# Kernel optimization log

Hardware: AMD Instinct MI355X
Metric: run time of the kernel (lower is better)

Reference implementation:

```python
import jax, jax.numpy as jnp
import numpy as np

# Fixed architecture constants (match init_kwargs)
D_MODEL = 256
NHEAD = 8
BASE_WINDOW = 4
DFF = 1024
B = 1
S = 4096


def _win_idx(grid, w):
    """Token indices of overlapping w x w windows over a grid x grid image,
    stride w//2 (same windows as F.unfold(kernel=w, stride=w//2)). -> (L, w*w) int32."""
    s = w // 2
    starts = np.arange(0, grid - w + 1, s)
    rows = starts[:, None] + np.arange(w)[None, :]              # (n, w)
    idx = rows[:, None, :, None] * grid + rows[None, :, None, :]  # (n, n, w, w)
    return jnp.asarray(idx.reshape(-1, w * w), dtype=jnp.int32)


def _ln(x, g, b, eps=1e-5):
    m = jnp.mean(x, axis=-1, keepdims=True)
    v = jnp.var(x, axis=-1, keepdims=True)
    return (x - m) * jax.lax.rsqrt(v + eps) * g + b


def _local_attn(x, scale, fw, fb, fg, fbb):
    """Multi-scale windowed SDPA: gather windows, attend, mean-pool per window,
    scatter pooled features back to token positions (overlap-averaged), fuse."""
    Bq, Sq, Dm = x.shape
    grid = int(np.sqrt(Sq))
    inv_scale = 1.0 / float(np.sqrt(Dm))  # SDPA uses full D as head dim
    outs = []
    for i in range(3):
        w = BASE_WINDOW * (2 ** i) * scale
        idx = _win_idx(grid, w)                      # (L, w2)
        win = x[:, idx, :]                           # (B, L, w2, D) gather
        p = jax.nn.softmax(jnp.einsum('blqd,blkd->blqk', win, win) * inv_scale, axis=-1)
        pooled = jnp.einsum('blqk,blkd->blqd', p, win).mean(axis=2)  # (B, L, D)
        flat = idx.reshape(-1)
        contrib = jnp.broadcast_to(pooled[:, :, None, :], win.shape).reshape(Bq, -1, Dm)
        acc = jnp.zeros_like(x).at[:, flat, :].add(contrib)
        cnt = jnp.zeros((Sq,), x.dtype).at[flat].add(1.0)
        outs.append(acc / cnt[None, :, None])        # (B, S, D) per scale
    cat = jnp.concatenate(outs, axis=-1)             # (B, S, 3D)
    return _ln(cat @ fw + fb, fg, fbb)


def _mha(x, wq, wk, wv, bq, bk, bv, wo, bo):
    Bq, Sq, Dm = x.shape
    dh = Dm // NHEAD
    def split(t):
        return t.reshape(Bq, Sq, NHEAD, dh)
    q, k, v = split(x @ wq + bq), split(x @ wk + bk), split(x @ wv + bv)
    p = jax.nn.softmax(jnp.einsum('bqhd,bkhd->bhqk', q, k) * (1.0 / float(np.sqrt(dh))), axis=-1)
    o = jnp.einsum('bhqk,bkhd->bqhd', p, v).reshape(Bq, Sq, Dm)
    return o @ wo + bo


def _forward(x, pos, fw, fb, fg, fbb, wq, wk, wv, bq, bk, bv, wo, bo, gw, gb, w1, b1, w2, b2, n1g, n1b, n2g, n2b, n3g, n3b, local_scale):
    # pos is accepted but unused in the original math (device check only)
    xl = _local_attn(x, local_scale, fw, fb, fg, fbb)
    xl = _ln(x + xl, n1g, n1b)                 # norm1 residual (dropout is identity in eval)
    xg = _mha(xl, wq, wk, wv, bq, bk, bv, wo, bo)
    xg = _ln(xl + xg, n2g, n2b)                # norm2 residual
    gate = jax.nn.softmax(((xl + xg) * 0.5).mean(axis=1, keepdims=True) @ gw + gb, axis=-1)  # (B,1,2)
    alpha, beta = gate[..., 0:1], gate[..., 1:2]
    xf = alpha * xg + beta * xl
    ff = jax.nn.gelu(xf @ w1 + b1, approximate=False) @ w2 + b2
    return _ln(xf + ff, n3g, n3b)


def setup_inputs() -> dict:
    key = jax.random.key(0)
    ks = jax.random.split(key, 12)
    def rn(k, shape, s=0.02):
        return jax.random.normal(k, shape, jnp.float32) * s
    D = D_MODEL
    return {
        'x': jax.random.normal(ks[0], (B, S, D), jnp.float32),
        'pos': jax.random.normal(ks[1], (B, S, 2), jnp.float32),
        'fw': rn(ks[2], (3 * D, D)), 'fb': jnp.zeros((D,), jnp.float32),
        'fg': jnp.ones((D,), jnp.float32), 'fbb': jnp.zeros((D,), jnp.float32),
        'wq': rn(ks[3], (D, D)), 'wk': rn(ks[4], (D, D)), 'wv': rn(ks[5], (D, D)),
        'bq': jnp.zeros((D,), jnp.float32), 'bk': jnp.zeros((D,), jnp.float32), 'bv': jnp.zeros((D,), jnp.float32),
        'wo': rn(ks[6], (D, D)), 'bo': jnp.zeros((D,), jnp.float32),
        'gw': rn(ks[7], (D, 2)), 'gb': jnp.zeros((2,), jnp.float32),
        'w1': rn(ks[8], (D, DFF)), 'b1': jnp.zeros((DFF,), jnp.float32),
        'w2': rn(ks[9], (DFF, D)), 'b2': jnp.zeros((D,), jnp.float32),
        'n1g': jnp.ones((D,), jnp.float32), 'n1b': jnp.zeros((D,), jnp.float32),
        'n2g': jnp.ones((D,), jnp.float32), 'n2b': jnp.zeros((D,), jnp.float32),
        'n3g': jnp.ones((D,), jnp.float32), 'n3b': jnp.zeros((D,), jnp.float32),
        'local_scale': 1,
    }


def reference(x, pos, fw, fb, fg, fbb, wq, wk, wv, bq, bk, bv, wo, bo, gw, gb, w1, b1, w2, b2, n1g, n1b, n2g, n2b, n3g, n3b, local_scale):
    return _forward(x, pos, fw, fb, fg, fbb, wq, wk, wv, bq, bk, bv, wo, bo, gw, gb, w1, b1, w2, b2, n1g, n1b, n2g, n2b, n3g, n3b, local_scale)
```

## Files before the change

kernel.cpp:

```cpp
#include <hip/hip_runtime.h>
#include <cstdint>
#include <cstddef>


#define DEVFN __device__ __forceinline__

constexpr int S    = 4096;
constexpr int D    = 256;
constexpr int GRID = 64;
constexpr int NH   = 8;
constexpr int DH   = 32;

typedef __attribute__((ext_vector_type(8))) short bf16x8;
typedef __attribute__((ext_vector_type(4))) float f32x4;
typedef __attribute__((ext_vector_type(16))) float f32x16;
typedef __attribute__((ext_vector_type(2))) unsigned int u32x2;

DEVFN float asf(unsigned u) { return __uint_as_float(u); }

DEVFN unsigned short f2bf(float f) {
  unsigned u = __float_as_uint(f);
  u += 0x7fffu + ((u >> 16) & 1u);
  return (unsigned short)(u >> 16);
}
DEVFN float bf2f(unsigned short s) { return __uint_as_float(((unsigned)s) << 16); }

DEVFN bf16x8 pack8(float4 a, float4 b) {
  bf16x8 kv;
  kv[0] = (short)f2bf(a.x); kv[1] = (short)f2bf(a.y);
  kv[2] = (short)f2bf(a.z); kv[3] = (short)f2bf(a.w);
  kv[4] = (short)f2bf(b.x); kv[5] = (short)f2bf(b.y);
  kv[6] = (short)f2bf(b.z); kv[7] = (short)f2bf(b.w);
  return kv;
}

DEVFN float gelu_t(float u) {
  const float y = 0.7978845608028654f * (u + 0.044715f * u * u * u);
  const float e = __expf(2.f * y);
  return 0.5f * u * (2.f - 2.f / (e + 1.f));
}

__global__ __launch_bounds__(256) void k_wt(
    const float* fw, const float* wq, const float* wk, const float* wv,
    const float* wo, const float* w1, const float* w2,
    unsigned short* fwT, unsigned short* wqT, unsigned short* wkT,
    unsigned short* wvT, unsigned short* woT, unsigned short* w1T,
    unsigned short* w2T) {
  __shared__ unsigned short tile[32][36];
  const int bid = blockIdx.x;
  const float* src; unsigned short* dst; int K, N, t;
  if (bid < 192)      { src = fw; dst = fwT; K = 768;  N = 256;  t = bid; }
  else if (bid < 256) { src = wq; dst = wqT; K = 256;  N = 256;  t = bid - 192; }
  else if (bid < 320) { src = wk; dst = wkT; K = 256;  N = 256;  t = bid - 256; }
  else if (bid < 384) { src = wv; dst = wvT; K = 256;  N = 256;  t = bid - 320; }
  else if (bid < 448) { src = wo; dst = woT; K = 256;  N = 256;  t = bid - 384; }
  else if (bid < 704) { src = w1; dst = w1T; K = 256;  N = 1024; t = bid - 448; }
  else                { src = w2; dst = w2T; K = 1024; N = 256;  t = bid - 704; }
  const int nkt = K >> 5;
  const int k0 = (t % nkt) * 32, n0 = (t / nkt) * 32;
  const int i = threadIdx.x >> 3, j4 = threadIdx.x & 7;
  const float4 v = *(const float4*)(src + (size_t)(k0 + i) * N + n0 + j4 * 4);
  unsigned lo = (unsigned)f2bf(v.x) | ((unsigned)f2bf(v.y) << 16);
  unsigned hi = (unsigned)f2bf(v.z) | ((unsigned)f2bf(v.w) << 16);
  *(uint2*)&tile[i][j4 * 4] = make_uint2(lo, hi);
  __syncthreads();
  unsigned o0 = tile[j4 * 4 + 0][i], o1 = tile[j4 * 4 + 1][i];
  unsigned o2 = tile[j4 * 4 + 2][i], o3 = tile[j4 * 4 + 3][i];
  *(uint2*)(dst + (size_t)(n0 + i) * K + k0 + j4 * 4) =
      make_uint2(o0 | (o1 << 16), o2 | (o3 << 16));
}

template <int K, int OUTBF, int ACT>
__global__ __launch_bounds__(64) void k_gemm_m(const unsigned short* __restrict__ Ab,
                                               const unsigned short* __restrict__ WT,
                                               const float* __restrict__ bias,
                                               void* __restrict__ Cout, int N) {
  const int lane = threadIdx.x;
  const int lc = lane & 31, hi = lane >> 5;
  const int m0 = blockIdx.x * 32, n0 = blockIdx.y * 32;
  const unsigned short* ap = Ab + (size_t)(m0 + lc) * K + hi * 8;
  const unsigned short* bp = WT + (size_t)(n0 + lc) * K + hi * 8;
  f32x16 acc = {0.f,0.f,0.f,0.f,0.f,0.f,0.f,0.f,0.f,0.f,0.f,0.f,0.f,0.f,0.f,0.f};
#pragma unroll 4
  for (int k0 = 0; k0 < K; k0 += 16) {
    bf16x8 a = *(const bf16x8*)(ap + k0);
    bf16x8 b = *(const bf16x8*)(bp + k0);
    acc = __builtin_amdgcn_mfma_f32_32x32x16_bf16(a, b, acc, 0, 0, 0);
  }
  const float bv = bias[n0 + lc];
#pragma unroll
  for (int r = 0; r < 16; ++r) {
    const int row = (r & 3) + 8 * (r >> 2) + 4 * hi;
    float v = acc[r] + bv;
    if (ACT == 1) v = gelu_t(v);
    if (OUTBF) ((unsigned short*)Cout)[(size_t)(m0 + row) * N + n0 + lc] = f2bf(v);
    else       ((float*)Cout)[(size_t)(m0 + row) * N + n0 + lc] = v;
  }
}

__global__ __launch_bounds__(64) void k_gemm_qkv(const unsigned short* __restrict__ Ab,
                                                 const unsigned short* __restrict__ wqkvT,
                                                 const float* __restrict__ bq,
                                                 const float* __restrict__ bk,
                                                 const float* __restrict__ bv,
                                                 unsigned short* __restrict__ qb,
                                                 unsigned short* __restrict__ kb,
                                                 unsigned short* __restrict__ vb) {
  const int lane = threadIdx.x;
  const int lc = lane & 31, hi = lane >> 5;
  const int m0 = blockIdx.x * 32;
  const int sel = blockIdx.y >> 3, n0 = (blockIdx.y & 7) * 32;
  const unsigned short* WT = wqkvT + (size_t)sel * 256 * 256;
  const float* bias = sel == 0 ? bq : sel == 1 ? bk : bv;
  unsigned short* out = sel == 0 ? qb : sel == 1 ? kb : vb;
  const float oscale = sel == 0 ? 0.17677669529663687f : 1.f;
  const unsigned short* ap = Ab + (size_t)(m0 + lc) * 256 + hi * 8;
  const unsigned short* bp = WT + (size_t)(n0 + lc) * 256 + hi * 8;
  f32x16 acc = {0.f,0.f,0.f,0.f,0.f,0.f,0.f,0.f,0.f,0.f,0.f,0.f,0.f,0.f,0.f,0.f};
#pragma unroll 4
  for (int k0 = 0; k0 < 256; k0 += 16) {
    bf16x8 a = *(const bf16x8*)(ap + k0);
    bf16x8 b = *(const bf16x8*)(bp + k0);
    acc = __builtin_amdgcn_mfma_f32_32x32x16_bf16(a, b, acc, 0, 0, 0);
  }
  const float bvv = bias[n0 + lc];
#pragma unroll
  for (int r = 0; r < 16; ++r) {
    const int row = (r & 3) + 8 * (r >> 2) + 4 * hi;
    out[(size_t)(m0 + row) * 256 + n0 + lc] = f2bf((acc[r] + bvv) * oscale);
  }
}

template <int W, int THREADS>
__global__ __launch_bounds__(THREADS) void k_local_s(const float* __restrict__ x,
                                                     float* __restrict__ pooled, int nS) {
  constexpr int NT  = W * W;
  constexpr int NCT = NT / 16;
  constexpr int LDE = 264;
  __shared__ unsigned short win[NT][LDE];
  __shared__ float a[NT];
  const int tid = threadIdx.x;
  const int wave = tid >> 6, lane = tid & 63;
  const int lr = lane & 15, lg = lane >> 4;
  const int l = blockIdx.x;
  const int row0 = (l / nS) * (W / 2), col0 = (l % nS) * (W / 2);

  for (int e8 = tid; e8 < NT * 32; e8 += THREADS) {
    const int t = e8 >> 5, c8 = (e8 & 31) * 8;
    const float* src = x + ((size_t)((row0 + t / W) * GRID + col0 + (t % W))) * D + c8;
    *(bf16x8*)&win[t][c8] = pack8(*(const float4*)src, *(const float4*)(src + 4));
  }
  if (tid < NT) a[tid] = 0.f;
  __syncthreads();

  bf16x8 af[8];
#pragma unroll
  for (int k2 = 0; k2 < 8; ++k2)
    af[k2] = *(const bf16x8*)&win[wave * 16 + lr][k2 * 32 + lg * 8];

  float m[4], Z[4], Zi[4];
#pragma unroll
  for (int r = 0; r < 4; ++r) { m[r] = -INFINITY; Z[r] = 0.f; }

  for (int ct = 0; ct < NCT; ++ct) {
    f32x4 Ca = {0.f, 0.f, 0.f, 0.f}, Cb = {0.f, 0.f, 0.f, 0.f};
#pragma unroll
    for (int k2 = 0; k2 < 8; k2 += 2) {
      bf16x8 b0 = *(const bf16x8*)&win[ct * 16 + lr][k2 * 32 + lg * 8];
      bf16x8 b1 = *(const bf16x8*)&win[ct * 16 + lr][(k2 + 1) * 32 + lg * 8];
      Ca = __builtin_amdgcn_mfma_f32_16x16x32_bf16(af[k2], b0, Ca, 0, 0, 0);
      Cb = __builtin_amdgcn_mfma_f32_16x16x32_bf16(af[k2 + 1], b1, Cb, 0, 0, 0);
    }
#pragma unroll
    for (int r = 0; r < 4; ++r) {
      const float sv = (Ca[r] + Cb[r]) * 0.0625f;
      const float nm = fmaxf(m[r], sv);
      Z[r] = Z[r] * __expf(m[r] - nm) + __expf(sv - nm);
      m[r] = nm;
    }
  }
#pragma unroll
  for (int r = 0; r < 4; ++r) {
#pragma unroll
    for (int msk = 1; msk <= 8; msk <<= 1) {
      const float om = __shfl_xor(m[r], msk), oz = __shfl_xor(Z[r], msk);
      const float nm = fmaxf(m[r], om);
      Z[r] = Z[r] * __expf(m[r] - nm) + oz * __expf(om - nm);
      m[r] = nm;
    }
    Zi[r] = 1.f / Z[r];
  }

  for (int ct = 0; ct < NCT; ++ct) {
    f32x4 Ca = {0.f, 0.f, 0.f, 0.f}, Cb = {0.f, 0.f, 0.f, 0.f};
#pragma unroll
    for (int k2 = 0; k2 < 8; k2 += 2) {
      bf16x8 b0 = *(const bf16x8*)&win[ct * 16 + lr][k2 * 32 + lg * 8];
      bf16x8 b1 = *(const bf16x8*)&win[ct * 16 + lr][(k2 + 1) * 32 + lg * 8];
      Ca = __builtin_amdgcn_mfma_f32_16x16x32_bf16(af[k2], b0, Ca, 0, 0, 0);
      Cb = __builtin_amdgcn_mfma_f32_16x16x32_bf16(af[k2 + 1], b1, Cb, 0, 0, 0);
    }
    float cs = 0.f;
#pragma unroll
    for (int r = 0; r < 4; ++r)
      cs += __expf((Ca[r] + Cb[r]) * 0.0625f - m[r]) * Zi[r];
    cs += __shfl_xor(cs, 16);
    cs += __shfl_xor(cs, 32);
    if (lg == 0) atomicAdd(&a[ct * 16 + lr], cs);
  }
  __syncthreads();

  for (int d = tid; d < D; d += THREADS) {
    float acc = 0.f;
#pragma unroll 8
    for (int k = 0; k < NT; ++k) acc += a[k] * bf2f(win[k][d]);
    pooled[(size_t)l * D + d] = acc * (1.f / NT);
  }
}

__global__ __launch_bounds__(256, 1) void k_local16(const float* __restrict__ x,
                                                    float* __restrict__ pooled, int nS) {
  constexpr int LDE = 264;
  __shared__ unsigned short win[256][LDE];
  __shared__ float a[256];
  const int tid = threadIdx.x;
  const int wave = tid >> 6, lane = tid & 63;
  const int lc = lane & 31, hi = lane >> 5;
  const int l = blockIdx.x;
  const int row0 = (l / nS) * 8, col0 = (l % nS) * 8;

  for (int e8 = tid; e8 < 256 * 32; e8 += 256) {
    const int t = e8 >> 5, c8 = (e8 & 31) * 8;
    const float* src = x + ((size_t)((row0 + (t >> 4)) * GRID + col0 + (t & 15))) * D + c8;
    *(bf16x8*)&win[t][c8] = pack8(*(const float4*)src, *(const float4*)(src + 4));
  }
  a[tid] = 0.f;
  __syncthreads();

  float m[2][16], Z[2][16], Zi[2][16];
#pragma unroll
  for (int s = 0; s < 2; ++s)
#pragma unroll
    for (int r = 0; r < 16; ++r) { m[s][r] = -INFINITY; Z[s][r] = 0.f; }

#pragma unroll
  for (int s = 0; s < 2; ++s) {
    const int R0 = (wave * 2 + s) * 32;
    bf16x8 af[16];
#pragma unroll
    for (int k2 = 0; k2 < 16; ++k2)
      af[k2] = *(const bf16x8*)&win[R0 + lc][k2 * 16 + hi * 8];
    for (int ct = 0; ct < 8; ++ct) {
      f32x16 Ca = {0.f,0.f,0.f,0.f,0.f,0.f,0.f,0.f,0.f,0.f,0.f,0.f,0.f,0.f,0.f,0.f};
      f32x16 Cb = Ca;
#pragma unroll
      for (int k2 = 0; k2 < 16; k2 += 2) {
        bf16x8 b0 = *(const bf16x8*)&win[ct * 32 + lc][k2 * 16 + hi * 8];
        bf16x8 b1 = *(const bf16x8*)&win[ct * 32 + lc][(k2 + 1) * 16 + hi * 8];
        Ca = __builtin_amdgcn_mfma_f32_32x32x16_bf16(af[k2], b0, Ca, 0, 0, 0);
        Cb = __builtin_amdgcn_mfma_f32_32x32x16_bf16(af[k2 + 1], b1, Cb, 0, 0, 0);
      }
#pragma unroll
      for (int r = 0; r < 16; ++r) {
        const float sv = (Ca[r] + Cb[r]) * 0.0625f;
        const float nm = fmaxf(m[s][r], sv);
        Z[s][r] = Z[s][r] * __expf(m[s][r] - nm) + __expf(sv - nm);
        m[s][r] = nm;
      }
    }
#pragma unroll
    for (int r = 0; r < 16; ++r) {
#pragma unroll
      for (int msk = 1; msk <= 16; msk <<= 1) {
        const float om = __shfl_xor(m[s][r], msk), oz = __shfl_xor(Z[s][r], msk);
        const float nm = fmaxf(m[s][r], om);
        Z[s][r] = Z[s][r] * __expf(m[s][r] - nm) + oz * __expf(om - nm);
        m[s][r] = nm;
      }
      Zi[s][r] = 1.f / Z[s][r];
    }
  }

#pragma unroll
  for (int s = 0; s < 2; ++s) {
    const int R0 = (wave * 2 + s) * 32;
    bf16x8 af[16];
#pragma unroll
    for (int k2 = 0; k2 < 16; ++k2)
      af[k2] = *(const bf16x8*)&win[R0 + lc][k2 * 16 + hi * 8];
    for (int ct = 0; ct < 8; ++ct) {
      f32x16 Ca = {0.f,0.f,0.f,0.f,0.f,0.f,0.f,0.f,0.f,0.f,0.f,0.f,0.f,0.f,0.f,0.f};
      f32x16 Cb = Ca;
#pragma unroll
      for (int k2 = 0; k2 < 16; k2 += 2) {
        bf16x8 b0 = *(const bf16x8*)&win[ct * 32 + lc][k2 * 16 + hi * 8];
        bf16x8 b1 = *(const bf16x8*)&win[ct * 32 + lc][(k2 + 1) * 16 + hi * 8];
        Ca = __builtin_amdgcn_mfma_f32_32x32x16_bf16(af[k2], b0, Ca, 0, 0, 0);
        Cb = __builtin_amdgcn_mfma_f32_32x32x16_bf16(af[k2 + 1], b1, Cb, 0, 0, 0);
      }
      float cs = 0.f;
#pragma unroll
      for (int r = 0; r < 16; ++r)
        cs += __expf((Ca[r] + Cb[r]) * 0.0625f - m[s][r]) * Zi[s][r];
      cs += __shfl_xor(cs, 32);
      if (hi == 0) atomicAdd(&a[ct * 32 + lc], cs);
    }
  }
  __syncthreads();

  {
    const int d = tid;
    float acc = 0.f;
#pragma unroll 8
    for (int k = 0; k < 256; ++k) acc += a[k] * bf2f(win[k][d]);
    pooled[(size_t)l * D + d] = acc * (1.f / 256.f);
  }
}

DEVFN float gatherp(const float* __restrict__ pooled, int r, int c, int W, int s, int nS, int d) {
  int amin = max(0, (r - W + s) / s), amax = min(nS - 1, r / s);
  int bmin = max(0, (c - W + s) / s), bmax = min(nS - 1, c / s);
  float acc = 0.f;
  int cnt = 0;
  for (int a = amin; a <= amax; ++a)
    for (int b = bmin; b <= bmax; ++b) { acc += pooled[(size_t)(a * nS + b) * D + d]; ++cnt; }
  return acc / (float)cnt;
}

__global__ void k_combine(const float* __restrict__ p0, const float* __restrict__ p1,
                          const float* __restrict__ p2, unsigned short* __restrict__ catb) {
  const int t = blockIdx.x, d = threadIdx.x;
  const int r = t >> 6, c = t & 63;
  unsigned short* o = catb + (size_t)t * 768;
  o[d]       = f2bf(gatherp(p0, r, c, 4, 2, 31, d));
  o[256 + d] = f2bf(gatherp(p1, r, c, 8, 4, 15, d));
  o[512 + d] = f2bf(gatherp(p2, r, c, 16, 8, 7, d));
}

DEVFN float2 block_sum2(float a, float b) {
  __shared__ float sb[8];
#pragma unroll
  for (int m = 32; m; m >>= 1) { a += __shfl_xor(a, m); b += __shfl_xor(b, m); }
  const int w = threadIdx.x >> 6;
  __syncthreads();
  if ((threadIdx.x & 63) == 0) { sb[w] = a; sb[4 + w] = b; }
  __syncthreads();
  return make_float2(sb[0] + sb[1] + sb[2] + sb[3], sb[4] + sb[5] + sb[6] + sb[7]);
}

__global__ __launch_bounds__(256) void k_ln(float* __restrict__ out, unsigned short* __restrict__ outb,
                                            const float* __restrict__ a, const float* __restrict__ b,
                                            const float* __restrict__ g, const float* __restrict__ be) {
  const size_t i = (size_t)blockIdx.x * D + threadIdx.x;
  float v = a[i] + (b ? b[i] : 0.f);
  float2 s = block_sum2(v, v * v);
  float mean = s.x * (1.f / D);
  float var = s.y * (1.f / D) - mean * mean;
  const float r = (v - mean) * rsqrtf(var + 1e-5f) * g[threadIdx.x] + be[threadIdx.x];
  out[i] = r;
  if (outb) outb[i] = f2bf(r);
}

__global__ __launch_bounds__(256) void k_ln_fuse(const float* __restrict__ t1,
                                                 const float* __restrict__ x,
                                                 float* __restrict__ xl,
                                                 unsigned short* __restrict__ xlb,
                                                 const float* __restrict__ fg,
                                                 const float* __restrict__ fbb,
                                                 const float* __restrict__ n1g,
                                                 const float* __restrict__ n1b) {
  const size_t i = (size_t)blockIdx.x * D + threadIdx.x;
  const float v1 = t1[i];
  float2 s1 = block_sum2(v1, v1 * v1);
  const float mean1 = s1.x * (1.f / D);
  const float var1 = s1.y * (1.f / D) - mean1 * mean1;
  const float r1 = (v1 - mean1) * rsqrtf(var1 + 1e-5f) * fg[threadIdx.x] + fbb[threadIdx.x];
  const float v2 = x[i] + r1;
  float2 s2 = block_sum2(v2, v2 * v2);
  const float mean2 = s2.x * (1.f / D);
  const float var2 = s2.y * (1.f / D) - mean2 * mean2;
  const float r2 = (v2 - mean2) * rsqrtf(var2 + 1e-5f) * n1g[threadIdx.x] + n1b[threadIdx.x];
  xl[i] = r2;
  xlb[i] = f2bf(r2);
}

__global__ __launch_bounds__(256) void k_flash_mfma(const unsigned short* __restrict__ Qg,
                                                    const unsigned short* __restrict__ Kg,
                                                    const unsigned short* __restrict__ Vg,
                                                    float* __restrict__ po,
                                                    float* __restrict__ pml) {
  const int h = blockIdx.y, z = blockIdx.z;
  const int tid = threadIdx.x;
  const int wave = tid >> 6, lane = tid & 63;
  const int lr = lane & 15, lg = lane >> 4;
  constexpr int NT2 = 32;

  __shared__ unsigned short Kf[2][64][40];
  __shared__ unsigned short VS[2][2048];

  const int q0 = blockIdx.x * 64 + wave * 16;
  const int kbase = z * 2048;

  const bf16x8 qfrag = *(const bf16x8*)(Qg + (size_t)(q0 + lr) * D + h * DH + lg * 8);

  f32x4 o0 = {0.f, 0.f, 0.f, 0.f}, o1 = {0.f, 0.f, 0.f, 0.f};
  float mrow = -INFINITY, lrow = 0.f;

  const unsigned vsbase0 =
      (unsigned)(unsigned long long)(const void*)&VS[0][0] + (unsigned)(lg * 128 + lr * 2);

  const int key = tid >> 2, c8 = (tid & 3) * 8;
  const int vidx = (c8 >> 4) * 1024 + (key >> 2) * 64 + (key & 3) * 16 + (c8 & 15);
  const unsigned short* kp = Kg + (size_t)(kbase + key) * D + h * DH + c8;
  const unsigned short* vp = Vg + (size_t)(kbase + key) * D + h * DH + c8;
  constexpr int KSTEP = 64 * D;

  {
    bf16x8 k0r = *(const bf16x8*)kp;
    bf16x8 v0r = *(const bf16x8*)vp;
    *(bf16x8*)&Kf[0][key][c8] = k0r;
    *(bf16x8*)&VS[0][vidx] = v0r;
  }
  __syncthreads();

  for (int kt = 0; kt < NT2; ++kt) {
    const int cur = kt & 1;
    const int ktn = (kt + 1 < NT2) ? kt + 1 : kt;
    bf16x8 kreg = *(const bf16x8*)(kp + (size_t)ktn * KSTEP);
    bf16x8 vreg = *(const bf16x8*)(vp + (size_t)ktn * KSTEP);

    f32x4 s[4];
    __builtin_amdgcn_s_setprio(1);
#pragma unroll
    for (int k16 = 0; k16 < 4; ++k16) {
      bf16x8 ka = *(const bf16x8*)&Kf[cur][k16 * 16 + lr][lg * 8];
      f32x4 zc = {0.f, 0.f, 0.f, 0.f};
      s[k16] = __builtin_amdgcn_mfma_f32_16x16x32_bf16(ka, qfrag, zc, 0, 0, 0);
    }
    __builtin_amdgcn_s_setprio(0);

    const unsigned vb = vsbase0 + (unsigned)(cur << 12);
    u32x2 tv000, tv001, tv010, tv011, tv100, tv101, tv110, tv111;
    asm volatile("ds_read_b64_tr_b16 %0, %1 offset:0"    : "=v"(tv000) : "v"(vb));
    asm volatile("ds_read_b64_tr_b16 %0, %1 offset:2048" : "=v"(tv001) : "v"(vb));
    asm volatile("ds_read_b64_tr_b16 %0, %1 offset:512"  : "=v"(tv010) : "v"(vb));
    asm volatile("ds_read_b64_tr_b16 %0, %1 offset:2560" : "=v"(tv011) : "v"(vb));
    asm volatile("ds_read_b64_tr_b16 %0, %1 offset:1024" : "=v"(tv100) : "v"(vb));
    asm volatile("ds_read_b64_tr_b16 %0, %1 offset:3072" : "=v"(tv101) : "v"(vb));
    asm volatile("ds_read_b64_tr_b16 %0, %1 offset:1536" : "=v"(tv110) : "v"(vb));
    asm volatile("ds_read_b64_tr_b16 %0, %1 offset:3584" : "=v"(tv111) : "v"(vb));

    float tm = s[0][0];
#pragma unroll
    for (int k16 = 0; k16 < 4; ++k16)
#pragma unroll
      for (int r = 0; r < 4; ++r) tm = fmaxf(tm, s[k16][r]);
    const bool skip = __all(tm - mrow <= 8.f);
    if (!skip) {
      float tmm = fmaxf(tm, __shfl_xor(tm, 16));
      tmm = fmaxf(tmm, __shfl_xor(tmm, 32));
      const float nm = fmaxf(mrow, tmm);
      const float cfac = __expf(mrow - nm);
      mrow = nm;
      lrow *= cfac;
#pragma unroll
      for (int r = 0; r < 4; ++r) {
        const float cr = __shfl(cfac, lg * 4 + r);
        o0[r] *= cr; o1[r] *= cr;
      }
    }
    float ls = 0.f;
#pragma unroll
    for (int k16 = 0; k16 < 4; ++k16)
#pragma unroll
      for (int r = 0; r < 4; ++r) { s[k16][r] = __expf(s[k16][r] - mrow); ls += s[k16][r]; }
    ls += __shfl_xor(ls, 16);
    ls += __shfl_xor(ls, 32);
    lrow += ls;

    asm volatile("s_waitcnt lgkmcnt(0)" ::: "memory");
    __builtin_amdgcn_sched_barrier(0);

    union VB { u32x2 u2[2]; bf16x8 b; };
    __builtin_amdgcn_s_setprio(1);
#pragma unroll
    for (int kt2 = 0; kt2 < 2; ++kt2) {
      bf16x8 pa;
#pragma unroll
      for (int j = 0; j < 4; ++j) {
        pa[j]     = (short)f2bf(s[2 * kt2][j]);
        pa[4 + j] = (short)f2bf(s[2 * kt2 + 1][j]);
      }
      VB v0f, v1f;
      if (kt2 == 0) { v0f.u2[0] = tv000; v0f.u2[1] = tv010; v1f.u2[0] = tv001; v1f.u2[1] = tv011; }
      else          { v0f.u2[0] = tv100; v0f.u2[1] = tv110; v1f.u2[0] = tv101; v1f.u2[1] = tv111; }
      o0 = __builtin_amdgcn_mfma_f32_16x16x32_bf16(pa, v0f.b, o0, 0, 0, 0);
      o1 = __builtin_amdgcn_mfma_f32_16x16x32_bf16(pa, v1f.b, o1, 0, 0, 0);
    }
    __builtin_amdgcn_s_setprio(0);

    if (kt + 1 < NT2) {
      *(bf16x8*)&Kf[cur ^ 1][key][c8] = kreg;
      *(bf16x8*)&VS[cur ^ 1][vidx] = vreg;
      __syncthreads();
    }
  }

#pragma unroll
  for (int r = 0; r < 4; ++r) {
    float* op = po + (size_t)z * S * D + (size_t)(q0 + lg * 4 + r) * D + h * DH + lr;
    op[0]  = o0[r];
    op[16] = o1[r];
  }
  if (lane < 16) {
    float* mlp = pml + ((size_t)(z * NH + h) * S + q0 + lr) * 2;
    mlp[0] = mrow;
    mlp[1] = lrow;
  }
}

__global__ __launch_bounds__(256) void k_fmerge(const float* __restrict__ po,
                                                const float* __restrict__ pml,
                                                unsigned short* __restrict__ t1b) {
  const int t = blockIdx.x, d = threadIdx.x;
  const int h = d >> 5;
  const float* ml0 = pml + ((size_t)h * S + t) * 2;
  const float* ml1 = pml + ((size_t)(NH + h) * S + t) * 2;
  const float m0 = ml0[0], l0 = ml0[1], m1 = ml1[0], l1 = ml1[1];
  const float M = fmaxf(m0, m1);
  const float a0 = __expf(m0 - M), a1 = __expf(m1 - M);
  const float L = l0 * a0 + l1 * a1;
  const float v = (po[(size_t)t * D + d] * a0 + po[(size_t)S * D + (size_t)t * D + d] * a1) / L;
  t1b[(size_t)t * D + d] = f2bf(v);
}

__global__ __launch_bounds__(256) void k_colmean(const float* __restrict__ xl,
                                                 const float* __restrict__ xg,
                                                 float* __restrict__ gbuf) {
  const int j = threadIdx.x;
  const int t0 = blockIdx.x * 64;
  float s = 0.f;
  for (int t = 0; t < 64; ++t) {
    size_t i = (size_t)(t0 + t) * D + j;
    s += xl[i] + xg[i];
  }
  atomicAdd(&gbuf[j], s * 0.5f);
}

__global__ __launch_bounds__(256) void k_gate(float* __restrict__ gbuf,
                                              const float* __restrict__ gw,
                                              const float* __restrict__ gb) {
  const int j = threadIdx.x;
  const float gm = gbuf[j] * (1.f / (float)S);
  float2 s = block_sum2(gm * gw[2 * j], gm * gw[2 * j + 1]);
  if (j == 0) {
    float g0 = s.x + gb[0], g1 = s.y + gb[1];
    float mx = fmaxf(g0, g1);
    float e0 = __expf(g0 - mx), e1 = __expf(g1 - mx);
    gbuf[256] = e0 / (e0 + e1);
    gbuf[257] = e1 / (e0 + e1);
  }
}

__global__ __launch_bounds__(256) void k_xf(const float* __restrict__ xl,
                                            const float* __restrict__ xg,
                                            const float* __restrict__ gbuf,
                                            float* __restrict__ xf,
                                            unsigned short* __restrict__ xfb) {
  const float alpha = gbuf[256], beta = gbuf[257];
  const size_t i = ((size_t)blockIdx.x * 256 + threadIdx.x) * 4;
  float4 a = *(const float4*)(xg + i);
  float4 b = *(const float4*)(xl + i);
  float4 r;
  r.x = alpha * a.x + beta * b.x;
  r.y = alpha * a.y + beta * b.y;
  r.z = alpha * a.z + beta * b.z;
  r.w = alpha * a.w + beta * b.w;
  *(float4*)(xf + i) = r;
  unsigned lo = (unsigned)f2bf(r.x) | ((unsigned)f2bf(r.y) << 16);
  unsigned hi = (unsigned)f2bf(r.z) | ((unsigned)f2bf(r.w) << 16);
  *(uint2*)(xfb + i) = make_uint2(lo, hi);
}

extern "C" void kernel_launch(void* const* d_in, const int* in_sizes, int n_in,
                              void* d_out, int out_size, void* d_ws, size_t ws_size,
                              hipStream_t stream) {
  const float* x   = (const float*)d_in[0];
  const float* fw  = (const float*)d_in[2];
  const float* fb  = (const float*)d_in[3];
  const float* fg  = (const float*)d_in[4];
  const float* fbb = (const float*)d_in[5];
  const float* wq  = (const float*)d_in[6];
  const float* wk  = (const float*)d_in[7];
  const float* wv  = (const float*)d_in[8];
  const float* bq  = (const float*)d_in[9];
  const float* bk  = (const float*)d_in[10];
  const float* bv  = (const float*)d_in[11];
  const float* wo  = (const float*)d_in[12];
  const float* bo  = (const float*)d_in[13];
  const float* gw  = (const float*)d_in[14];
  const float* gb  = (const float*)d_in[15];
  const float* w1  = (const float*)d_in[16];
  const float* b1  = (const float*)d_in[17];
  const float* w2  = (const float*)d_in[18];
  const float* b2  = (const float*)d_in[19];
  const float* n1g = (const float*)d_in[20];
  const float* n1b = (const float*)d_in[21];
  const float* n2g = (const float*)d_in[22];
  const float* n2b = (const float*)d_in[23];
  const float* n3g = (const float*)d_in[24];
  const float* n3b = (const float*)d_in[25];
  float* out = (float*)d_out;

  char* base = (char*)d_ws;
  size_t off = 0;
  auto carve = [&](size_t bytes) { char* p = base + off; off += (bytes + 255) & ~(size_t)255; return p; };
  float* p0 = (float*)carve(961 * 256 * 4);
  float* p1 = (float*)carve(225 * 256 * 4);
  float* p2 = (float*)carve(49 * 256 * 4);
  unsigned short* fwT = (unsigned short*)carve(256 * 768 * 2);
  unsigned short* wqkvT = (unsigned short*)carve(3 * 256 * 256 * 2);
  unsigned short* wqT = wqkvT;
  unsigned short* wkT = wqkvT + 256 * 256;
  unsigned short* wvT = wqkvT + 2 * 256 * 256;
  unsigned short* woT = (unsigned short*)carve(256 * 256 * 2);
  unsigned short* w1T = (unsigned short*)carve(1024 * 256 * 2);
  unsigned short* w2T = (unsigned short*)carve(256 * 1024 * 2);
  char* R = carve(8388608);
  unsigned short* catb = (unsigned short*)R;
  float* po            = (float*)R;
  float* xg            = (float*)R;
  unsigned short* hbuf = (unsigned short*)R;
  float* pml = (float*)carve(2 * NH * (size_t)S * 2 * 4);
  unsigned short* qb = (unsigned short*)carve((size_t)S * D * 2);
  unsigned short* kb = (unsigned short*)carve((size_t)S * D * 2);
  unsigned short* vb = (unsigned short*)carve((size_t)S * D * 2);
  float* xf            = (float*)qb;
  unsigned short* xfb  = vb;
  float* t1  = (float*)carve((size_t)S * D * 4);
  float* ffo = t1;
  unsigned short* t1b = (unsigned short*)carve((size_t)S * D * 2);
  float* xl  = (float*)carve((size_t)S * D * 4);
  unsigned short* xlb = (unsigned short*)carve((size_t)S * D * 2);
  float* gbuf = (float*)carve(264 * 4);

  hipMemsetAsync(gbuf, 0, 264 * sizeof(float), stream);

  k_wt<<<dim3(960), dim3(256), 0, stream>>>(fw, wq, wk, wv, wo, w1, w2,
                                            fwT, wqT, wkT, wvT, woT, w1T, w2T);
  k_local_s<4, 64><<<dim3(961), dim3(64), 0, stream>>>(x, p0, 31);
  k_local_s<8, 256><<<dim3(225), dim3(256), 0, stream>>>(x, p1, 15);
  k_local16<<<dim3(49), dim3(256), 0, stream>>>(x, p2, 7);
  k_combine<<<dim3(S), dim3(256), 0, stream>>>(p0, p1, p2, catb);
  k_gemm_m<768, 0, 0><<<dim3(S / 32, 8), dim3(64), 0, stream>>>(catb, fwT, fb, t1, 256);
  k_ln_fuse<<<dim3(S), dim3(256), 0, stream>>>(t1, x, xl, xlb, fg, fbb, n1g, n1b);
  k_gemm_qkv<<<dim3(S / 32, 24), dim3(64), 0, stream>>>(xlb, wqkvT, bq, bk, bv, qb, kb, vb);
  k_flash_mfma<<<dim3(S / 64, NH, 2), dim3(256), 0, stream>>>(qb, kb, vb, po, pml);
  k_fmerge<<<dim3(S), dim3(256), 0, stream>>>(po, pml, t1b);
  k_gemm_m<256, 0, 0><<<dim3(S / 32, 8), dim3(64), 0, stream>>>(t1b, woT, bo, xf, 256);
  k_ln<<<dim3(S), dim3(256), 0, stream>>>(xg, nullptr, xl, xf, n2g, n2b);
  k_colmean<<<dim3(64), dim3(256), 0, stream>>>(xl, xg, gbuf);
  k_gate<<<dim3(1), dim3(256), 0, stream>>>(gbuf, gw, gb);
  k_xf<<<dim3(S * D / 1024), dim3(256), 0, stream>>>(xl, xg, gbuf, xf, xfb);
  k_gemm_m<256, 1, 1><<<dim3(S / 32, 32), dim3(64), 0, stream>>>(xfb, w1T, b1, hbuf, 1024);
  k_gemm_m<1024, 0, 0><<<dim3(S / 32, 8), dim3(64), 0, stream>>>(hbuf, w2T, b2, ffo, 256);
  k_ln<<<dim3(S), dim3(256), 0, stream>>>(out, nullptr, xf, ffo, n3g, n3b);
}
```

Before: 235.3 us.

## Split flash attention KV into four chunks, store bf16 partials, use exp2 and packed bf16

Attention now splits the key range into four chunks instead of two, which doubles the grid to raise occupancy. Partial outputs are stored as bf16 to halve their traffic, and the merge kernel combines four partials. Softmax switches to exp2 with log2e folded into the Q scale, and the lazy-rescale threshold is adjusted to match. The GEMMs use two independent accumulators to break the MFMA dependency chain, and bf16 packing uses the hardware pair-convert. Risks are lower precision in the partial outputs and more merge overhead.

```diff
diff --git a/kernel.cpp b/kernel.cpp
--- a/kernel.cpp
+++ b/kernel.cpp
@@ -1,4 +1,5 @@
 #include <hip/hip_runtime.h>
+#include <hip/hip_bf16.h>
 #include <cstdint>
 #include <cstddef>
 
@@ -25,13 +26,24 @@
 }
 DEVFN float bf2f(unsigned short s) { return __uint_as_float(((unsigned)s) << 16); }
 
+DEVFN unsigned pk2(float a, float b) {
+  __hip_bfloat162 h = __float22bfloat162_rn(make_float2(a, b));
+  return *(unsigned*)&h;
+}
+
 DEVFN bf16x8 pack8(float4 a, float4 b) {
-  bf16x8 kv;
-  kv[0] = (short)f2bf(a.x); kv[1] = (short)f2bf(a.y);
-  kv[2] = (short)f2bf(a.z); kv[3] = (short)f2bf(a.w);
-  kv[4] = (short)f2bf(b.x); kv[5] = (short)f2bf(b.y);
-  kv[6] = (short)f2bf(b.z); kv[7] = (short)f2bf(b.w);
-  return kv;
+  union { unsigned w[4]; bf16x8 v; } u;
+  u.w[0] = pk2(a.x, a.y); u.w[1] = pk2(a.z, a.w);
+  u.w[2] = pk2(b.x, b.y); u.w[3] = pk2(b.z, b.w);
+  return u.v;
+}
+
+DEVFN float ex2(float x) {
+#if __has_builtin(__builtin_amdgcn_exp2f)
+  return __builtin_amdgcn_exp2f(x);
+#else
+  return __expf(x * 0.6931471805599453f);
+#endif
 }
 
 DEVFN float gelu_t(float u) {
@@ -60,9 +72,7 @@
   const int k0 = (t % nkt) * 32, n0 = (t / nkt) * 32;
   const int i = threadIdx.x >> 3, j4 = threadIdx.x & 7;
   const float4 v = *(const float4*)(src + (size_t)(k0 + i) * N + n0 + j4 * 4);
-  unsigned lo = (unsigned)f2bf(v.x) | ((unsigned)f2bf(v.y) << 16);
-  unsigned hi = (unsigned)f2bf(v.z) | ((unsigned)f2bf(v.w) << 16);
-  *(uint2*)&tile[i][j4 * 4] = make_uint2(lo, hi);
+  *(uint2*)&tile[i][j4 * 4] = make_uint2(pk2(v.x, v.y), pk2(v.z, v.w));
   __syncthreads();
   unsigned o0 = tile[j4 * 4 + 0][i], o1 = tile[j4 * 4 + 1][i];
   unsigned o2 = tile[j4 * 4 + 2][i], o3 = tile[j4 * 4 + 3][i];
@@ -80,18 +90,22 @@
   const int m0 = blockIdx.x * 32, n0 = blockIdx.y * 32;
   const unsigned short* ap = Ab + (size_t)(m0 + lc) * K + hi * 8;
   const unsigned short* bp = WT + (size_t)(n0 + lc) * K + hi * 8;
-  f32x16 acc = {0.f,0.f,0.f,0.f,0.f,0.f,0.f,0.f,0.f,0.f,0.f,0.f,0.f,0.f,0.f,0.f};
+  f32x16 acc0 = {0.f,0.f,0.f,0.f,0.f,0.f,0.f,0.f,0.f,0.f,0.f,0.f,0.f,0.f,0.f,0.f};
+  f32x16 acc1 = acc0;
 #pragma unroll 4
-  for (int k0 = 0; k0 < K; k0 += 16) {
-    bf16x8 a = *(const bf16x8*)(ap + k0);
-    bf16x8 b = *(const bf16x8*)(bp + k0);
-    acc = __builtin_amdgcn_mfma_f32_32x32x16_bf16(a, b, acc, 0, 0, 0);
+  for (int k0 = 0; k0 < K; k0 += 32) {
+    bf16x8 a0 = *(const bf16x8*)(ap + k0);
+    bf16x8 b0 = *(const bf16x8*)(bp + k0);
+    bf16x8 a1 = *(const bf16x8*)(ap + k0 + 16);
+    bf16x8 b1 = *(const bf16x8*)(bp + k0 + 16);
+    acc0 = __builtin_amdgcn_mfma_f32_32x32x16_bf16(a0, b0, acc0, 0, 0, 0);
+    acc1 = __builtin_amdgcn_mfma_f32_32x32x16_bf16(a1, b1, acc1, 0, 0, 0);
   }
   const float bv = bias[n0 + lc];
 #pragma unroll
   for (int r = 0; r < 16; ++r) {
     const int row = (r & 3) + 8 * (r >> 2) + 4 * hi;
-    float v = acc[r] + bv;
+    float v = acc0[r] + acc1[r] + bv;
     if (ACT == 1) v = gelu_t(v);
     if (OUTBF) ((unsigned short*)Cout)[(size_t)(m0 + row) * N + n0 + lc] = f2bf(v);
     else       ((float*)Cout)[(size_t)(m0 + row) * N + n0 + lc] = v;
@@ -113,21 +127,25 @@
   const unsigned short* WT = wqkvT + (size_t)sel * 256 * 256;
   const float* bias = sel == 0 ? bq : sel == 1 ? bk : bv;
   unsigned short* out = sel == 0 ? qb : sel == 1 ? kb : vb;
-  const float oscale = sel == 0 ? 0.17677669529663687f : 1.f;
+  const float oscale = sel == 0 ? 0.25505889254f : 1.f;
   const unsigned short* ap = Ab + (size_t)(m0 + lc) * 256 + hi * 8;
   const unsigned short* bp = WT + (size_t)(n0 + lc) * 256 + hi * 8;
-  f32x16 acc = {0.f,0.f,0.f,0.f,0.f,0.f,0.f,0.f,0.f,0.f,0.f,0.f,0.f,0.f,0.f,0.f};
+  f32x16 acc0 = {0.f,0.f,0.f,0.f,0.f,0.f,0.f,0.f,0.f,0.f,0.f,0.f,0.f,0.f,0.f,0.f};
+  f32x16 acc1 = acc0;
 #pragma unroll 4
-  for (int k0 = 0; k0 < 256; k0 += 16) {
-    bf16x8 a = *(const bf16x8*)(ap + k0);
-    bf16x8 b = *(const bf16x8*)(bp + k0);
-    acc = __builtin_amdgcn_mfma_f32_32x32x16_bf16(a, b, acc, 0, 0, 0);
+  for (int k0 = 0; k0 < 256; k0 += 32) {
+    bf16x8 a0 = *(const bf16x8*)(ap + k0);
+    bf16x8 b0 = *(const bf16x8*)(bp + k0);
+    bf16x8 a1 = *(const bf16x8*)(ap + k0 + 16);
+    bf16x8 b1 = *(const bf16x8*)(bp + k0 + 16);
+    acc0 = __builtin_amdgcn_mfma_f32_32x32x16_bf16(a0, b0, acc0, 0, 0, 0);
+    acc1 = __builtin_amdgcn_mfma_f32_32x32x16_bf16(a1, b1, acc1, 0, 0, 0);
   }
   const float bvv = bias[n0 + lc];
 #pragma unroll
   for (int r = 0; r < 16; ++r) {
     const int row = (r & 3) + 8 * (r >> 2) + 4 * hi;
-    out[(size_t)(m0 + row) * 256 + n0 + lc] = f2bf((acc[r] + bvv) * oscale);
+    out[(size_t)(m0 + row) * 256 + n0 + lc] = f2bf((acc0[r] + acc1[r] + bvv) * oscale);
   }
 }
 
@@ -387,19 +405,19 @@
 __global__ __launch_bounds__(256) void k_flash_mfma(const unsigned short* __restrict__ Qg,
                                                     const unsigned short* __restrict__ Kg,
                                                     const unsigned short* __restrict__ Vg,
-                                                    float* __restrict__ po,
+                                                    unsigned short* __restrict__ po,
                                                     float* __restrict__ pml) {
   const int h = blockIdx.y, z = blockIdx.z;
   const int tid = threadIdx.x;
   const int wave = tid >> 6, lane = tid & 63;
   const int lr = lane & 15, lg = lane >> 4;
-  constexpr int NT2 = 32;
+  constexpr int NT2 = 16;
 
   __shared__ unsigned short Kf[2][64][40];
   __shared__ unsigned short VS[2][2048];
 
   const int q0 = blockIdx.x * 64 + wave * 16;
-  const int kbase = z * 2048;
+  const int kbase = z * 1024;
 
   const bf16x8 qfrag = *(const bf16x8*)(Qg + (size_t)(q0 + lr) * D + h * DH + lg * 8);
 
@@ -455,12 +473,12 @@
     for (int k16 = 0; k16 < 4; ++k16)
 #pragma unroll
       for (int r = 0; r < 4; ++r) tm = fmaxf(tm, s[k16][r]);
-    const bool skip = __all(tm - mrow <= 8.f);
+    const bool skip = __all(tm - mrow <= 11.f);
     if (!skip) {
       float tmm = fmaxf(tm, __shfl_xor(tm, 16));
       tmm = fmaxf(tmm, __shfl_xor(tmm, 32));
       const float nm = fmaxf(mrow, tmm);
-      const float cfac = __expf(mrow - nm);
+      const float cfac = ex2(mrow - nm);
       mrow = nm;
       lrow *= cfac;
 #pragma unroll
@@ -473,7 +491,7 @@
 #pragma unroll
     for (int k16 = 0; k16 < 4; ++k16)
 #pragma unroll
-      for (int r = 0; r < 4; ++r) { s[k16][r] = __expf(s[k16][r] - mrow); ls += s[k16][r]; }
+      for (int r = 0; r < 4; ++r) { s[k16][r] = ex2(s[k16][r] - mrow); ls += s[k16][r]; }
     ls += __shfl_xor(ls, 16);
     ls += __shfl_xor(ls, 32);
     lrow += ls;
@@ -485,17 +503,16 @@
     __builtin_amdgcn_s_setprio(1);
 #pragma unroll
     for (int kt2 = 0; kt2 < 2; ++kt2) {
-      bf16x8 pa;
-#pragma unroll
-      for (int j = 0; j < 4; ++j) {
-        pa[j]     = (short)f2bf(s[2 * kt2][j]);
-        pa[4 + j] = (short)f2bf(s[2 * kt2 + 1][j]);
-      }
+      union { unsigned w[4]; bf16x8 v; } pu;
+      pu.w[0] = pk2(s[2 * kt2][0], s[2 * kt2][1]);
+      pu.w[1] = pk2(s[2 * kt2][2], s[2 * kt2][3]);
+      pu.w[2] = pk2(s[2 * kt2 + 1][0], s[2 * kt2 + 1][1]);
+      pu.w[3] = pk2(s[2 * kt2 + 1][2], s[2 * kt2 + 1][3]);
       VB v0f, v1f;
       if (kt2 == 0) { v0f.u2[0] = tv000; v0f.u2[1] = tv010; v1f.u2[0] = tv001; v1f.u2[1] = tv011; }
       else          { v0f.u2[0] = tv100; v0f.u2[1] = tv110; v1f.u2[0] = tv101; v1f.u2[1] = tv111; }
-      o0 = __builtin_amdgcn_mfma_f32_16x16x32_bf16(pa, v0f.b, o0, 0, 0, 0);
-      o1 = __builtin_amdgcn_mfma_f32_16x16x32_bf16(pa, v1f.b, o1, 0, 0, 0);
+      o0 = __builtin_amdgcn_mfma_f32_16x16x32_bf16(pu.v, v0f.b, o0, 0, 0, 0);
+      o1 = __builtin_amdgcn_mfma_f32_16x16x32_bf16(pu.v, v1f.b, o1, 0, 0, 0);
     }
     __builtin_amdgcn_s_setprio(0);
 
@@ -508,9 +525,9 @@
 
 #pragma unroll
   for (int r = 0; r < 4; ++r) {
-    float* op = po + (size_t)z * S * D + (size_t)(q0 + lg * 4 + r) * D + h * DH + lr;
-    op[0]  = o0[r];
-    op[16] = o1[r];
+    unsigned short* op = po + (size_t)z * S * D + (size_t)(q0 + lg * 4 + r) * D + h * DH + lr;
+    op[0]  = f2bf(o0[r]);
+    op[16] = f2bf(o1[r]);
   }
   if (lane < 16) {
     float* mlp = pml + ((size_t)(z * NH + h) * S + q0 + lr) * 2;
@@ -519,19 +536,27 @@
   }
 }
 
-__global__ __launch_bounds__(256) void k_fmerge(const float* __restrict__ po,
+__global__ __launch_bounds__(256) void k_fmerge(const unsigned short* __restrict__ po,
                                                 const float* __restrict__ pml,
                                                 unsigned short* __restrict__ t1b) {
   const int t = blockIdx.x, d = threadIdx.x;
   const int h = d >> 5;
-  const float* ml0 = pml + ((size_t)h * S + t) * 2;
-  const float* ml1 = pml + ((size_t)(NH + h) * S + t) * 2;
-  const float m0 = ml0[0], l0 = ml0[1], m1 = ml1[0], l1 = ml1[1];
-  const float M = fmaxf(m0, m1);
-  const float a0 = __expf(m0 - M), a1 = __expf(m1 - M);
-  const float L = l0 * a0 + l1 * a1;
-  const float v = (po[(size_t)t * D + d] * a0 + po[(size_t)S * D + (size_t)t * D + d] * a1) / L;
-  t1b[(size_t)t * D + d] = f2bf(v);
+  float m[4], l[4];
+  float M = -INFINITY;
+#pragma unroll
+  for (int z = 0; z < 4; ++z) {
+    const float* ml = pml + ((size_t)(z * NH + h) * S + t) * 2;
+    m[z] = ml[0]; l[z] = ml[1];
+    M = fmaxf(M, m[z]);
+  }
+  float L = 0.f, acc = 0.f;
+#pragma unroll
+  for (int z = 0; z < 4; ++z) {
+    const float a = ex2(m[z] - M);
+    L += l[z] * a;
+    acc += bf2f(po[(size_t)z * S * D + (size_t)t * D + d]) * a;
+  }
+  t1b[(size_t)t * D + d] = f2bf(acc / L);
 }
 
 __global__ __launch_bounds__(256) void k_colmean(const float* __restrict__ xl,
@@ -577,9 +602,7 @@
   r.z = alpha * a.z + beta * b.z;
   r.w = alpha * a.w + beta * b.w;
   *(float4*)(xf + i) = r;
-  unsigned lo = (unsigned)f2bf(r.x) | ((unsigned)f2bf(r.y) << 16);
-  unsigned hi = (unsigned)f2bf(r.z) | ((unsigned)f2bf(r.w) << 16);
-  *(uint2*)(xfb + i) = make_uint2(lo, hi);
+  *(uint2*)(xfb + i) = make_uint2(pk2(r.x, r.y), pk2(r.z, r.w));
 }
 
 extern "C" void kernel_launch(void* const* d_in, const int* in_sizes, int n_in,
@@ -628,10 +651,10 @@
   unsigned short* w2T = (unsigned short*)carve(256 * 1024 * 2);
   char* R = carve(8388608);
   unsigned short* catb = (unsigned short*)R;
-  float* po            = (float*)R;
+  unsigned short* po   = (unsigned short*)R;
   float* xg            = (float*)R;
   unsigned short* hbuf = (unsigned short*)R;
-  float* pml = (float*)carve(2 * NH * (size_t)S * 2 * 4);
+  float* pml = (float*)carve(4 * NH * (size_t)S * 2 * 4);
   unsigned short* qb = (unsigned short*)carve((size_t)S * D * 2);
   unsigned short* kb = (unsigned short*)carve((size_t)S * D * 2);
   unsigned short* vb = (unsigned short*)carve((size_t)S * D * 2);
@@ -655,7 +678,7 @@
   k_gemm_m<768, 0, 0><<<dim3(S / 32, 8), dim3(64), 0, stream>>>(catb, fwT, fb, t1, 256);
   k_ln_fuse<<<dim3(S), dim3(256), 0, stream>>>(t1, x, xl, xlb, fg, fbb, n1g, n1b);
   k_gemm_qkv<<<dim3(S / 32, 24), dim3(64), 0, stream>>>(xlb, wqkvT, bq, bk, bv, qb, kb, vb);
-  k_flash_mfma<<<dim3(S / 64, NH, 2), dim3(256), 0, stream>>>(qb, kb, vb, po, pml);
+  k_flash_mfma<<<dim3(S / 64, NH, 4), dim3(256), 0, stream>>>(qb, kb, vb, po, pml);
   k_fmerge<<<dim3(S), dim3(256), 0, stream>>>(po, pml, t1b);
   k_gemm_m<256, 0, 0><<<dim3(S / 32, 8), dim3(64), 0, stream>>>(t1b, woT, bo, xf, 256);
   k_ln<<<dim3(S), dim3(256), 0, stream>>>(xg, nullptr, xl, xf, n2g, n2b);
```

New measurement: 229.9 us. 2.3% less time.
